# Performance work log

Hardware: AMD Instinct MI355X
Metric: run time of the kernel (lower is better)

Reference implementation:

```python
import jax, jax.numpy as jnp
import numpy as np

EPS_BN = 1e-5
NEG_SLOPE = 0.2

def gat_layer(x, src, dst, N, W, a_src, a_dst, b, heads, ch, concat):
    # x: [N, Fin]; W: [Fin, heads*ch]; a_src/a_dst: [heads, ch]; b: [heads*ch] or [ch]
    xw = (x @ W).reshape(N, heads, ch)                      # [N,H,C]
    al_src = jnp.einsum('nhc,hc->nh', xw, a_src)            # [N,H]
    al_dst = jnp.einsum('nhc,hc->nh', xw, a_dst)
    e = jax.nn.leaky_relu(al_src[src] + al_dst[dst], NEG_SLOPE)  # [E,H]
    m = jax.ops.segment_max(e, dst, num_segments=N)         # segment softmax (stable)
    ee = jnp.exp(e - m[dst])
    s = jax.ops.segment_sum(ee, dst, num_segments=N)
    alpha = ee / (s[dst] + 1e-16)                            # [E,H]
    msg = xw[src] * alpha[:, :, None]                        # [E,H,C]
    out = jax.ops.segment_sum(msg, dst, num_segments=N)      # [N,H,C]
    if concat:
        return out.reshape(N, heads * ch) + b
    return out.mean(axis=1) + b

def setup_inputs():
    key = jax.random.key(0)
    ks = jax.random.split(key, 24)
    N, E, dim_in, dim_out = 20000, 320000, 256, 16
    x = jax.random.normal(ks[0], (N, dim_in), dtype=jnp.float32)
    edge_index = jax.random.randint(ks[1], (2, E), 0, N, dtype=jnp.int64)
    def glorot(k, shape):
        fan = shape[0] + shape[-1]
        return jax.random.uniform(k, shape, jnp.float32, -1.0, 1.0) * np.sqrt(6.0 / fan)
    return {
        'x': x, 'edge_index': edge_index,
        'bn_gamma': jnp.ones((dim_in,), jnp.float32),
        'bn_beta': jnp.zeros((dim_in,), jnp.float32),
        'W1': glorot(ks[2], (dim_in, 16 * 64)),
        'a1_src': glorot(ks[3], (16, 64)), 'a1_dst': glorot(ks[4], (16, 64)),
        'b1': jnp.zeros((16 * 64,), jnp.float32),
        'p1': jnp.float32(0.25),
        'W2': glorot(ks[5], (dim_in + 16 * 64, 8 * 8)),
        'a2_src': glorot(ks[6], (8, 8)), 'a2_dst': glorot(ks[7], (8, 8)),
        'b2': jnp.zeros((8 * 8,), jnp.float32),
        'p2': jnp.float32(0.25),
        'W3': glorot(ks[8], (8 * 8, 8 * dim_out)),
        'a3_src': glorot(ks[9], (8, dim_out)), 'a3_dst': glorot(ks[10], (8, dim_out)),
        'b3': jnp.zeros((dim_out,), jnp.float32),
    }

def reference(x, edge_index, bn_gamma, bn_beta, W1, a1_src, a1_dst, b1, p1,
              W2, a2_src, a2_dst, b2, p2, W3, a3_src, a3_dst, b3):
    N = x.shape[0]
    # PyG GATConv default add_self_loops=True
    loops = jnp.arange(N, dtype=edge_index.dtype)
    src = jnp.concatenate([edge_index[0], loops])
    dst = jnp.concatenate([edge_index[1], loops])
    # BatchNorm1d (training-mode batch stats)
    mu = x.mean(axis=0)
    var = x.var(axis=0)
    x_in = (x - mu) * jax.lax.rsqrt(var + EPS_BN) * bn_gamma + bn_beta
    h = gat_layer(x_in, src, dst, N, W1, a1_src, a1_dst, b1, 16, 64, True)
    h = jnp.where(h >= 0, h, p1 * h)  # PReLU
    h = gat_layer(jnp.concatenate([x_in, h], axis=1), src, dst, N, W2, a2_src, a2_dst, b2, 8, 8, True)
    h = jnp.where(h >= 0, h, p2 * h)
    h = gat_layer(h, src, dst, N, W3, a3_src, a3_dst, b3, 8, b3.shape[0], False)
    return jax.nn.log_softmax(h, axis=1)
```

## Files before the change

kernel.cpp:

```cpp
#include <hip/hip_runtime.h>
#include <math.h>

typedef unsigned int u32;
typedef unsigned short u16;
typedef u32 u32x4 __attribute__((ext_vector_type(4)));
typedef float f32x4 __attribute__((ext_vector_type(4)));

__device__ __forceinline__ u16 f2bf(float f) {
  u32 u = __builtin_bit_cast(u32, f);
  return (u16)((u + 0x7FFFu + ((u >> 16) & 1u)) >> 16);
}
__device__ __forceinline__ float bf2f(u32 lo16) {
  return __builtin_bit_cast(float, lo16 << 16);
}
__device__ __forceinline__ void mfma16(f32x4& c, const u32x4& a, const u32x4& b) {
  asm volatile("v_mfma_f32_16x16x32_bf16 %0, %1, %2, %0" : "+v"(c) : "v"(a), "v"(b));
}
__device__ __forceinline__ float lrelu(float e) { return fmaxf(e, 0.2f * e); }

__global__ void prep1_kernel(const float* __restrict__ x, float* __restrict__ musum,
                             float* __restrict__ sqsum, const int* __restrict__ ei, int E,
                             int N, int* __restrict__ cnt) {
  int b = blockIdx.x;
  int t = threadIdx.x;
  if (b < 256) {
    float s = 0.f, s2 = 0.f;
    for (int r = b; r < N; r += 256) {
      float v = x[(size_t)r * 256 + t];
      s += v;
      s2 += v * v;
    }
    atomicAdd(&musum[t], s);
    atomicAdd(&sqsum[t], s2);
  } else {
    int e = (b - 256) * 256 + t;
    int ET = E + N;
    if (e < ET) {
      int d = (e < E) ? ei[E + e] : (e - E);
      atomicAdd(&cnt[d], 1);
    }
  }
}

__global__ __launch_bounds__(1024) void prep2_kernel(
    int* __restrict__ cnt, int* __restrict__ row_ptr, int* __restrict__ perm,
    const float* __restrict__ x, const float* __restrict__ musum,
    const float* __restrict__ sqsum, const float* __restrict__ gamma,
    const float* __restrict__ beta, u16* __restrict__ xin, int N, float invN) {
  int t = threadIdx.x;
  if (blockIdx.x == 0) {
    __shared__ int part[1024];
    __shared__ int bins[256];
    __shared__ int bs[256];
    int chunk = (N + 1023) / 1024;
    int lo = min(t * chunk, N);
    int hi = min(lo + chunk, N);
    if (t < 256) bins[t] = 0;
    __syncthreads();
    int s = 0;
    for (int i = lo; i < hi; i++) {
      int d = cnt[i];
      s += d;
      atomicAdd(&bins[min(d, 255)], 1);
    }
    part[t] = s;
    __syncthreads();
    for (int off = 1; off < 1024; off <<= 1) {
      int v = (t >= off) ? part[t - off] : 0;
      __syncthreads();
      part[t] += v;
      __syncthreads();
    }
    if (t < 256) bs[t] = bins[t];
    __syncthreads();
    for (int off = 1; off < 256; off <<= 1) {
      int v = (t < 256 && t >= off) ? bs[t - off] : 0;
      __syncthreads();
      if (t < 256) bs[t] += v;
      __syncthreads();
    }
    if (t < 256) bins[t] = (t == 0) ? 0 : bs[t - 1];
    __syncthreads();
    for (int i = lo; i < hi; i++) {
      int d = min(cnt[i], 255);
      int pos = atomicAdd(&bins[d], 1);
      perm[pos] = i;
    }
    __syncthreads();
    int run = (t == 0) ? 0 : part[t - 1];
    for (int i = lo; i < hi; i++) {
      int d = cnt[i];
      row_ptr[i] = run;
      cnt[i] = run;
      run += d;
    }
    if (t == 1023) row_ptr[N] = part[1023];
  } else {
    int col = t & 255, ro = t >> 8;
    float mu = musum[col] * invN;
    float var = sqsum[col] * invN - mu * mu;
    float sc = gamma[col] * rsqrtf(var + 1e-5f);
    float sh = beta[col] - mu * sc;
    for (int r = (blockIdx.x - 1) * 4 + ro; r < N; r += 256 * 4) {
      size_t idx = (size_t)r * 256 + col;
      xin[idx] = f2bf(x[idx] * sc + sh);
    }
  }
}

__global__ void prep3_kernel(const int* __restrict__ ei, int E, int N, int FILLB,
                             int* __restrict__ cursor, int* __restrict__ csr_src,
                             const float* __restrict__ W1, const float* __restrict__ a1s,
                             const float* __restrict__ a1d, const float* __restrict__ W2,
                             const float* __restrict__ a2s, const float* __restrict__ a2d,
                             const float* __restrict__ W3, const float* __restrict__ a3s,
                             const float* __restrict__ a3d, u16* __restrict__ Wt1,
                             u16* __restrict__ Wt2, u16* __restrict__ Wt3) {
  int b = blockIdx.x;
  if (b < FILLB) {
    int e = b * 256 + threadIdx.x;
    int ET = E + N;
    if (e < ET) {
      int s, d;
      if (e < E) { s = ei[e]; d = ei[E + e]; }
      else       { s = e - E; d = s; }
      int pos = atomicAdd(&cursor[d], 1);
      csr_src[pos] = s;
    }
    return;
  }
  const int S1 = 1024 * 256, S2 = 64 * 1280, S3 = 128 * 64;
  const int A1 = 32 * 256, A2 = 16 * 1280, A3 = 16 * 64;
  const int Z1 = 96 * 256, Z2 = 16 * 1280, Z3 = 16 * 64;
  int o = (b - FILLB) * 256 + threadIdx.x;
  if (o < S1) {
    int n = o / 256, k = o % 256;
    Wt1[o] = f2bf(W1[(size_t)k * 1024 + n]);
    return;
  }
  o -= S1;
  if (o < S2) {
    int n = o / 1280, k = o % 1280;
    Wt2[o] = f2bf(W2[(size_t)k * 64 + n]);
    return;
  }
  o -= S2;
  if (o < S3) {
    int n = o / 64, k = o % 64;
    Wt3[o] = f2bf(W3[(size_t)k * 128 + n]);
    return;
  }
  o -= S3;
  if (o < A1) {
    int jj = o / 256, k = o % 256, h = jj >> 1;
    const float* av = (jj & 1) ? a1d : a1s;
    float s = 0.f;
    for (int c = 0; c < 64; c++) s += W1[(size_t)k * 1024 + h * 64 + c] * av[h * 64 + c];
    Wt1[(size_t)(1024 + jj) * 256 + k] = f2bf(s);
    return;
  }
  o -= A1;
  if (o < A2) {
    int jj = o / 1280, k = o % 1280, h = jj >> 1;
    const float* av = (jj & 1) ? a2d : a2s;
    float s = 0.f;
    for (int c = 0; c < 8; c++) s += W2[(size_t)k * 64 + h * 8 + c] * av[h * 8 + c];
    Wt2[(size_t)(64 + jj) * 1280 + k] = f2bf(s);
    return;
  }
  o -= A2;
  if (o < A3) {
    int jj = o / 64, k = o % 64, h = jj >> 1;
    const float* av = (jj & 1) ? a3d : a3s;
    float s = 0.f;
    for (int c = 0; c < 16; c++) s += W3[(size_t)k * 128 + h * 16 + c] * av[h * 16 + c];
    Wt3[(size_t)(128 + jj) * 64 + k] = f2bf(s);
    return;
  }
  o -= A3;
  if (o < Z1) { Wt1[1056 * 256 + o] = 0; return; }
  o -= Z1;
  if (o < Z2) { Wt2[80 * 1280 + o] = 0; return; }
  o -= Z2;
  if (o < Z3) { Wt3[144 * 64 + o] = 0; return; }
}

template <int BM, int BN, int FM, int FN>
__global__ __launch_bounds__(256) void mfma_gemm_al(
    const u16* __restrict__ A1, const u16* __restrict__ A2, int K1, int K,
    const u16* __restrict__ Wt, u16* __restrict__ Ch, int NcH,
    float* __restrict__ als, float* __restrict__ ald, int ALN, int ALP, int M) {
  constexpr int BK = 32;
  constexpr int ACH = (BM * BK) / 8;
  constexpr int BCH = (BN * BK) / 8;
  static_assert(BM == 2 * FM * 16 && BN == 2 * FN * 16, "wave grid 2x2");
  __shared__ u16 As[2][BM * BK];
  __shared__ u16 Bs[2][BN * BK];
  int t = threadIdx.x;
  int m0 = blockIdx.x * BM, n0 = blockIdx.y * BN;
  int r = t & 15;
  int g = (t >> 4) & 3;
  int wid = t >> 6;
  int wm0 = (wid >> 1) * (FM * 16);
  int wn0 = (wid & 1) * (FN * 16);
  int K8 = K >> 3;
  int K2 = K - K1;

  auto stage = [&](int buf, int k0) {
    const u16* Aseg;
    int sA, kl;
    if (k0 < K1) { Aseg = A1; sA = K1; kl = k0; }
    else         { Aseg = A2; sA = K2; kl = k0 - K1; }
#pragma unroll
    for (int i = 0; i < (ACH + 255) / 256; i++) {
      int c = i * 256 + t;
      if (ACH % 256 == 0 || c < ACH) {
        int m = c >> 2, kb = c & 3;
        __builtin_amdgcn_global_load_lds(
            (const __attribute__((address_space(1))) void*)(Aseg + (size_t)(m0 + m) * sA + kl + kb * 8),
            (__attribute__((address_space(3))) void*)(&As[buf][c * 8]), 16, 0, 0);
      }
    }
#pragma unroll
    for (int i = 0; i < (BCH + 255) / 256; i++) {
      int c = i * 256 + t;
      if (BCH % 256 == 0 || c < BCH) {
        int nn = c >> 2, kb = c & 3;
        __builtin_amdgcn_global_load_lds(
            (const __attribute__((address_space(1))) void*)(Wt + ((size_t)(n0 + nn) * K8 + (k0 >> 3) + kb) * 8),
            (__attribute__((address_space(3))) void*)(&Bs[buf][c * 8]), 16, 0, 0);
      }
    }
  };

  f32x4 acc[FM][FN] = {};
  asm volatile("s_nop 7\n\ts_nop 7" :::);

  stage(0, 0);
  __syncthreads();
  int nt = K / BK;
  for (int ts = 0; ts < nt; ts++) {
    if (ts + 1 < nt) stage((ts + 1) & 1, (ts + 1) * BK);
    int cur = ts & 1;
    u32x4 af[FM], bfr[FN];
#pragma unroll
    for (int fi = 0; fi < FM; fi++)
      af[fi] = *(const u32x4*)(&As[cur][((wm0 + fi * 16 + r) * 4 + g) * 8]);
#pragma unroll
    for (int fj = 0; fj < FN; fj++)
      bfr[fj] = *(const u32x4*)(&Bs[cur][((wn0 + fj * 16 + r) * 4 + g) * 8]);
#pragma unroll
    for (int fi = 0; fi < FM; fi++)
#pragma unroll
      for (int fj = 0; fj < FN; fj++) mfma16(acc[fi][fj], af[fi], bfr[fj]);
    __syncthreads();
  }
  asm volatile("s_nop 7\n\ts_nop 7" :::);

#pragma unroll
  for (int fi = 0; fi < FM; fi++) {
#pragma unroll
    for (int fj = 0; fj < FN; fj++) {
#pragma unroll
      for (int v = 0; v < 4; v++) {
        int m = m0 + wm0 + fi * 16 + g * 4 + v;
        int nn = n0 + wn0 + fj * 16 + r;
        if (m < M) {
          float val = acc[fi][fj][v];
          if (nn < NcH) {
            Ch[(size_t)m * NcH + nn] = f2bf(val);
          } else {
            int j = nn - NcH;
            if (j < ALN) ((j & 1) ? ald : als)[(size_t)(j >> 1) * ALP + m] = val;
          }
        }
      }
    }
  }
}

__global__ __launch_bounds__(256) void gat_agg1_gs(
    const u16* __restrict__ xwh, const float* __restrict__ alsrc,
    const float* __restrict__ aldst, const int* __restrict__ row_ptr,
    const int* __restrict__ csr_src, const int* __restrict__ perm,
    const float* __restrict__ bias, const float* __restrict__ slope_p,
    u16* __restrict__ out, int N, int ALP, int NBH) {
  constexpr int U = 4;
  int b = blockIdx.x;
  int xcd = b & 7, seq = b >> 3;
  int phase = seq / NBH, nb = seq - phase * NBH;
  int h = xcd + (phase << 3);
  int lane = threadIdx.x & 63;
  int g = lane >> 3, l8 = lane & 7;
  int ti = nb * 32 + (threadIdx.x >> 6) * 8 + g;
  int n = perm[min(ti, N - 1)];
  const float* alh = alsrc + (size_t)h * ALP;
  float ad = aldst[(size_t)h * ALP + n];
  int start = row_ptr[n];
  int end = row_ptr[n + 1];
  int deg = (ti < N) ? end - start : 0;
  int endm1 = end - 1;

  float m = -1e30f, s = 0.f;
  float acc[8] = {};
  const u16* base = xwh + (size_t)h * 64 + (size_t)l8 * 8;

  auto fma8 = [&](const u32x4& v, float w) {
#pragma unroll
    for (int i = 0; i < 4; i++) {
      u32 u = v[i];
      acc[2 * i] = fmaf(w, bf2f(u & 0xffffu), acc[2 * i]);
      acc[2 * i + 1] = fmaf(w, bf2f(u >> 16), acc[2 * i + 1]);
    }
  };

  int c[U];
#pragma unroll
  for (int i = 0; i < U; i++) c[i] = csr_src[min(start + i, endm1)];
  int j = 0;
  for (; j + U <= deg; j += U) {
    u32x4 v[U];
    float e[U];
#pragma unroll
    for (int i = 0; i < U; i++) v[i] = *(const u32x4*)(base + (size_t)c[i] * 1024);
#pragma unroll
    for (int i = 0; i < U; i++) e[i] = lrelu(alh[c[i]] + ad);
#pragma unroll
    for (int i = 0; i < U; i++) c[i] = csr_src[min(start + j + U + i, endm1)];
    float mn = fmaxf(fmaxf(e[0], e[1]), fmaxf(e[2], e[3]));
    if (mn > m) {
      float sc = __expf(m - mn);
      s *= sc;
#pragma unroll
      for (int k = 0; k < 8; k++) acc[k] *= sc;
      m = mn;
    }
#pragma unroll
    for (int i = 0; i < U; i++) {
      float w = __expf(e[i] - m);
      s += w;
      fma8(v[i], w);
    }
  }
  for (int i = 0; j < deg; j++, i++) {
    u32x4 v = *(const u32x4*)(base + (size_t)c[i] * 1024);
    float e = lrelu(alh[c[i]] + ad);
    if (e > m) {
      float sc = __expf(m - e);
      s *= sc;
#pragma unroll
      for (int k = 0; k < 8; k++) acc[k] *= sc;
      m = e;
    }
    float w = __expf(e - m);
    s += w;
    fma8(v, w);
  }
  float rr = 1.f / (s + 1e-16f);

  if (ti < N) {
    float p = slope_p[0];
    u32 ow[4];
#pragma unroll
    for (int i = 0; i < 4; i++) {
      int cc = h * 64 + l8 * 8 + 2 * i;
      float v0 = acc[2 * i] * rr + bias[cc];
      float v1 = acc[2 * i + 1] * rr + bias[cc + 1];
      v0 = (v0 >= 0.f) ? v0 : p * v0;
      v1 = (v1 >= 0.f) ? v1 : p * v1;
      ow[i] = (u32)f2bf(v0) | ((u32)f2bf(v1) << 16);
    }
    *(u32x4*)(out + (size_t)n * 1024 + h * 64 + l8 * 8) = *(u32x4*)ow;
  }
}

__global__ __launch_bounds__(256) void gat_agg2_gs(
    const u16* __restrict__ xwh, const float* __restrict__ alsrc,
    const float* __restrict__ aldst, const int* __restrict__ row_ptr,
    const int* __restrict__ csr_src, const int* __restrict__ perm,
    const float* __restrict__ bias, const float* __restrict__ slope_p,
    u16* __restrict__ out, int N, int ALP) {
  constexpr int U = 4;
  int lane = threadIdx.x & 63;
  int g = lane >> 3, l8 = lane & 7;
  int ti = blockIdx.x * 32 + (threadIdx.x >> 6) * 8 + g;
  int n = perm[min(ti, N - 1)];
  const float* alh = alsrc + (size_t)l8 * ALP;
  float ad = aldst[(size_t)l8 * ALP + n];
  int start = row_ptr[n];
  int end = row_ptr[n + 1];
  int deg = (ti < N) ? end - start : 0;
  int endm1 = end - 1;

  float m = -1e30f, s = 0.f;
  float acc[8] = {};
  const u16* base = xwh + (size_t)l8 * 8;

  auto fma8 = [&](const u32x4& v, float w) {
#pragma unroll
    for (int i = 0; i < 4; i++) {
      u32 u = v[i];
      acc[2 * i] = fmaf(w, bf2f(u & 0xffffu), acc[2 * i]);
      acc[2 * i + 1] = fmaf(w, bf2f(u >> 16), acc[2 * i + 1]);
    }
  };

  int c[U];
#pragma unroll
  for (int i = 0; i < U; i++) c[i] = csr_src[min(start + i, endm1)];
  int j = 0;
  for (; j + U <= deg; j += U) {
    u32x4 v[U];
    float e[U];
#pragma unroll
    for (int i = 0; i < U; i++) v[i] = *(const u32x4*)(base + (size_t)c[i] * 64);
#pragma unroll
    for (int i = 0; i < U; i++) e[i] = lrelu(alh[c[i]] + ad);
#pragma unroll
    for (int i = 0; i < U; i++) c[i] = csr_src[min(start + j + U + i, endm1)];
    float mn = fmaxf(fmaxf(e[0], e[1]), fmaxf(e[2], e[3]));
    if (mn > m) {
      float sc = __expf(m - mn);
      s *= sc;
#pragma unroll
      for (int k = 0; k < 8; k++) acc[k] *= sc;
      m = mn;
    }
#pragma unroll
    for (int i = 0; i < U; i++) {
      float w = __expf(e[i] - m);
      s += w;
      fma8(v[i], w);
    }
  }
  for (int i = 0; j < deg; j++, i++) {
    u32x4 v = *(const u32x4*)(base + (size_t)c[i] * 64);
    float e = lrelu(alh[c[i]] + ad);
    if (e > m) {
      float sc = __expf(m - e);
      s *= sc;
#pragma unroll
      for (int k = 0; k < 8; k++) acc[k] *= sc;
      m = e;
    }
    float w = __expf(e - m);
    s += w;
    fma8(v, w);
  }
  float rr = 1.f / (s + 1e-16f);

  if (ti < N) {
    float p = slope_p[0];
    u32 ow[4];
#pragma unroll
    for (int i = 0; i < 4; i++) {
      int cc = l8 * 8 + 2 * i;
      float v0 = acc[2 * i] * rr + bias[cc];
      float v1 = acc[2 * i + 1] * rr + bias[cc + 1];
      v0 = (v0 >= 0.f) ? v0 : p * v0;
      v1 = (v1 >= 0.f) ? v1 : p * v1;
      ow[i] = (u32)f2bf(v0) | ((u32)f2bf(v1) << 16);
    }
    *(u32x4*)(out + (size_t)n * 64 + l8 * 8) = *(u32x4*)ow;
  }
}

__global__ __launch_bounds__(256) void gat_agg3_gs(
    const u16* __restrict__ xwh, const float* __restrict__ alsrc,
    const float* __restrict__ aldst, const int* __restrict__ row_ptr,
    const int* __restrict__ csr_src, const int* __restrict__ perm,
    const float* __restrict__ bias, float* __restrict__ out, int N, int ALP) {
  constexpr int U = 4;
  int lane = threadIdx.x & 63;
  int g = lane >> 4, l16 = lane & 15;
  int head = l16 >> 1;
  int ti = blockIdx.x * 16 + (threadIdx.x >> 6) * 4 + g;
  int n = perm[min(ti, N - 1)];
  const float* alh = alsrc + (size_t)head * ALP;
  float ad = aldst[(size_t)head * ALP + n];
  int start = row_ptr[n];
  int end = row_ptr[n + 1];
  int deg = (ti < N) ? end - start : 0;
  int endm1 = end - 1;

  float m = -1e30f, s = 0.f;
  float acc[8] = {};
  const u16* base = xwh + (size_t)l16 * 8;

  auto fma8 = [&](const u32x4& v, float w) {
#pragma unroll
    for (int i = 0; i < 4; i++) {
      u32 u = v[i];
      acc[2 * i] = fmaf(w, bf2f(u & 0xffffu), acc[2 * i]);
      acc[2 * i + 1] = fmaf(w, bf2f(u >> 16), acc[2 * i + 1]);
    }
  };

  int c[U];
#pragma unroll
  for (int i = 0; i < U; i++) c[i] = csr_src[min(start + i, endm1)];
  int j = 0;
  for (; j + U <= deg; j += U) {
    u32x4 v[U];
    float e[U];
#pragma unroll
    for (int i = 0; i < U; i++) v[i] = *(const u32x4*)(base + (size_t)c[i] * 128);
#pragma unroll
    for (int i = 0; i < U; i++) e[i] = lrelu(alh[c[i]] + ad);
#pragma unroll
    for (int i = 0; i < U; i++) c[i] = csr_src[min(start + j + U + i, endm1)];
    float mn = fmaxf(fmaxf(e[0], e[1]), fmaxf(e[2], e[3]));
    if (mn > m) {
      float sc = __expf(m - mn);
      s *= sc;
#pragma unroll
      for (int k = 0; k < 8; k++) acc[k] *= sc;
      m = mn;
    }
#pragma unroll
    for (int i = 0; i < U; i++) {
      float w = __expf(e[i] - m);
      s += w;
      fma8(v[i], w);
    }
  }
  for (int i = 0; j < deg; j++, i++) {
    u32x4 v = *(const u32x4*)(base + (size_t)c[i] * 128);
    float e = lrelu(alh[c[i]] + ad);
    if (e > m) {
      float sc = __expf(m - e);
      s *= sc;
#pragma unroll
      for (int k = 0; k < 8; k++) acc[k] *= sc;
      m = e;
    }
    float w = __expf(e - m);
    s += w;
    fma8(v, w);
  }
  float rr = 1.f / (s + 1e-16f);
#pragma unroll
  for (int k = 0; k < 8; k++) acc[k] *= rr;

#pragma unroll
  for (int st = 2; st <= 8; st <<= 1)
#pragma unroll
    for (int k = 0; k < 8; k++) acc[k] += __shfl_xor(acc[k], st);

  int half = l16 & 1;
  float v8[8];
  float mx = -1e30f;
#pragma unroll
  for (int k = 0; k < 8; k++) {
    v8[k] = acc[k] * 0.125f + bias[half * 8 + k];
    mx = fmaxf(mx, v8[k]);
  }
  mx = fmaxf(mx, __shfl_xor(mx, 1));
  float se = 0.f;
#pragma unroll
  for (int k = 0; k < 8; k++) se += __expf(v8[k] - mx);
  se += __shfl_xor(se, 1);
  float lse = mx + logf(se);
  if (ti < N && l16 < 2) {
    float4 o0 = make_float4(v8[0] - lse, v8[1] - lse, v8[2] - lse, v8[3] - lse);
    float4 o1 = make_float4(v8[4] - lse, v8[5] - lse, v8[6] - lse, v8[7] - lse);
    float* op = out + (size_t)n * 16 + half * 8;
    *(float4*)op = o0;
    *(float4*)(op + 4) = o1;
  }
}

extern "C" void kernel_launch(void* const* d_in, const int* in_sizes, int n_in,
                              void* d_out, int out_size, void* d_ws, size_t ws_size,
                              hipStream_t stream) {
  const float* x        = (const float*)d_in[0];
  const int*   ei       = (const int*)d_in[1];
  const float* bn_gamma = (const float*)d_in[2];
  const float* bn_beta  = (const float*)d_in[3];
  const float* W1       = (const float*)d_in[4];
  const float* a1s      = (const float*)d_in[5];
  const float* a1d      = (const float*)d_in[6];
  const float* b1       = (const float*)d_in[7];
  const float* p1       = (const float*)d_in[8];
  const float* W2       = (const float*)d_in[9];
  const float* a2s      = (const float*)d_in[10];
  const float* a2d      = (const float*)d_in[11];
  const float* b2       = (const float*)d_in[12];
  const float* p2       = (const float*)d_in[13];
  const float* W3       = (const float*)d_in[14];
  const float* a3s      = (const float*)d_in[15];
  const float* a3d      = (const float*)d_in[16];
  const float* b3       = (const float*)d_in[17];
  float* out = (float*)d_out;

  const int F  = in_sizes[2];
  const int N  = in_sizes[0] / F;
  const int E  = in_sizes[1] / 2;
  const int ET = E + N;
  const int MP = ((N + 127) / 128) * 128;

  size_t off = 0;
  auto alloc = [&](size_t bytes) -> char* {
    char* r = (char*)d_ws + off;
    off += (bytes + 255) & ~(size_t)255;
    return r;
  };
  float* musum   = (float*)alloc(F * 4);
  float* sqsum   = (float*)alloc(F * 4);
  int*   cursor  = (int*)alloc((size_t)N * 4);
  int*   row_ptr = (int*)alloc((size_t)(N + 1) * 4);
  int*   csr_src = (int*)alloc((size_t)ET * 4);
  int*   perm    = (int*)alloc((size_t)N * 4);
  float* al_s    = (float*)alloc((size_t)16 * MP * 4);
  float* al_d    = (float*)alloc((size_t)16 * MP * 4);
  u16*   Wt1     = (u16*)alloc((size_t)1152 * 256 * 2);
  u16*   Wt2     = (u16*)alloc((size_t)96 * 1280 * 2);
  u16*   Wt3     = (u16*)alloc((size_t)160 * 64 * 2);
  u16*   x_in_h  = (u16*)alloc((size_t)MP * 256 * 2);
  u16*   xw1h    = (u16*)alloc((size_t)MP * 1024 * 2);
  u16*   h1      = (u16*)alloc((size_t)MP * 1024 * 2);
  u16*   xw2h    = (u16*)alloc((size_t)MP * 64 * 2);
  u16*   h2h     = (u16*)alloc((size_t)MP * 64 * 2);
  u16*   xw3h    = (u16*)alloc((size_t)MP * 128 * 2);

  hipMemsetAsync(musum, 0, (size_t)2 * F * 4 + (size_t)N * 4, stream);

  int CNTB = (ET + 255) / 256;
  prep1_kernel<<<256 + CNTB, 256, 0, stream>>>(x, musum, sqsum, ei, E, N, cursor);

  prep2_kernel<<<257, 1024, 0, stream>>>(cursor, row_ptr, perm, x, musum, sqsum, bn_gamma,
                                         bn_beta, x_in_h, N, 1.0f / (float)N);

  {
    int total_wt = 1024 * 256 + 64 * 1280 + 128 * 64
                 + 32 * 256 + 16 * 1280 + 16 * 64
                 + 96 * 256 + 16 * 1280 + 16 * 64;
    int WTB = (total_wt + 255) / 256;
    prep3_kernel<<<CNTB + WTB, 256, 0, stream>>>(ei, E, N, CNTB, cursor, csr_src, W1, a1s, a1d,
                                                 W2, a2s, a2d, W3, a3s, a3d, Wt1, Wt2, Wt3);
  }

  {
    dim3 grid(MP / 128, 9);
    mfma_gemm_al<128, 128, 4, 4><<<grid, 256, 0, stream>>>(
        x_in_h, x_in_h, 256, 256, Wt1, xw1h, 1024, al_s, al_d, 32, MP, N);
    int NBH = (N + 31) / 32;
    gat_agg1_gs<<<8 * NBH * 2, 256, 0, stream>>>(xw1h, al_s, al_d, row_ptr, csr_src, perm, b1, p1,
                                                 h1, N, MP, NBH);
  }

  {
    dim3 grid((N + 63) / 64, 1);
    mfma_gemm_al<64, 96, 2, 3><<<grid, 256, 0, stream>>>(
        x_in_h, h1, 256, 1280, Wt2, xw2h, 64, al_s, al_d, 16, MP, N);
    gat_agg2_gs<<<(N + 31) / 32, 256, 0, stream>>>(xw2h, al_s, al_d, row_ptr, csr_src, perm, b2,
                                                   p2, h2h, N, MP);
  }

  {
    dim3 grid((N + 63) / 64, 1);
    mfma_gemm_al<64, 160, 2, 5><<<grid, 256, 0, stream>>>(
        h2h, h2h, 64, 64, Wt3, xw3h, 128, al_s, al_d, 16, MP, N);
    gat_agg3_gs<<<(N + 15) / 16, 256, 0, stream>>>(xw3h, al_s, al_d, row_ptr, csr_src, perm, b3,
                                                   out, N, MP);
  }
}
```

Before: 307.8 us.

## Parameterize GEMM K-tile, shrink layer-2 M-tile, use packed FMA in aggregation

```diff
diff --git a/kernel.cpp b/kernel.cpp
--- a/kernel.cpp
+++ b/kernel.cpp
@@ -5,16 +5,23 @@
 typedef unsigned short u16;
 typedef u32 u32x4 __attribute__((ext_vector_type(4)));
 typedef float f32x4 __attribute__((ext_vector_type(4)));
+typedef float f32x2 __attribute__((ext_vector_type(2)));
 
 __device__ __forceinline__ u16 f2bf(float f) {
   u32 u = __builtin_bit_cast(u32, f);
   return (u16)((u + 0x7FFFu + ((u >> 16) & 1u)) >> 16);
 }
-__device__ __forceinline__ float bf2f(u32 lo16) {
-  return __builtin_bit_cast(float, lo16 << 16);
-}
 __device__ __forceinline__ void mfma16(f32x4& c, const u32x4& a, const u32x4& b) {
   asm volatile("v_mfma_f32_16x16x32_bf16 %0, %1, %2, %0" : "+v"(c) : "v"(a), "v"(b));
+}
+__device__ __forceinline__ void pkfma(f32x2& acc, f32x2 val, f32x2 w) {
+  asm volatile("v_pk_fma_f32 %0, %1, %2, %0" : "+v"(acc) : "v"(val), "v"(w));
+}
+__device__ __forceinline__ f32x2 unpk(u32 u) {
+  f32x2 v;
+  v.x = __builtin_bit_cast(float, u << 16);
+  v.y = __builtin_bit_cast(float, u & 0xffff0000u);
+  return v;
 }
 __device__ __forceinline__ float lrelu(float e) { return fmaxf(e, 0.2f * e); }
 
@@ -185,12 +192,12 @@
   if (o < Z3) { Wt3[144 * 64 + o] = 0; return; }
 }
 
-template <int BM, int BN, int FM, int FN>
+template <int BM, int BN, int FM, int FN, int BK>
 __global__ __launch_bounds__(256) void mfma_gemm_al(
     const u16* __restrict__ A1, const u16* __restrict__ A2, int K1, int K,
     const u16* __restrict__ Wt, u16* __restrict__ Ch, int NcH,
     float* __restrict__ als, float* __restrict__ ald, int ALN, int ALP, int M) {
-  constexpr int BK = 32;
+  constexpr int KC8 = BK / 8;
   constexpr int ACH = (BM * BK) / 8;
   constexpr int BCH = (BN * BK) / 8;
   static_assert(BM == 2 * FM * 16 && BN == 2 * FN * 16, "wave grid 2x2");
@@ -215,7 +222,7 @@
     for (int i = 0; i < (ACH + 255) / 256; i++) {
       int c = i * 256 + t;
       if (ACH % 256 == 0 || c < ACH) {
-        int m = c >> 2, kb = c & 3;
+        int m = c / KC8, kb = c % KC8;
         __builtin_amdgcn_global_load_lds(
             (const __attribute__((address_space(1))) void*)(Aseg + (size_t)(m0 + m) * sA + kl + kb * 8),
             (__attribute__((address_space(3))) void*)(&As[buf][c * 8]), 16, 0, 0);
@@ -225,7 +232,7 @@
     for (int i = 0; i < (BCH + 255) / 256; i++) {
       int c = i * 256 + t;
       if (BCH % 256 == 0 || c < BCH) {
-        int nn = c >> 2, kb = c & 3;
+        int nn = c / KC8, kb = c % KC8;
         __builtin_amdgcn_global_load_lds(
             (const __attribute__((address_space(1))) void*)(Wt + ((size_t)(n0 + nn) * K8 + (k0 >> 3) + kb) * 8),
             (__attribute__((address_space(3))) void*)(&Bs[buf][c * 8]), 16, 0, 0);
@@ -242,17 +249,20 @@
   for (int ts = 0; ts < nt; ts++) {
     if (ts + 1 < nt) stage((ts + 1) & 1, (ts + 1) * BK);
     int cur = ts & 1;
-    u32x4 af[FM], bfr[FN];
-#pragma unroll
-    for (int fi = 0; fi < FM; fi++)
-      af[fi] = *(const u32x4*)(&As[cur][((wm0 + fi * 16 + r) * 4 + g) * 8]);
-#pragma unroll
-    for (int fj = 0; fj < FN; fj++)
-      bfr[fj] = *(const u32x4*)(&Bs[cur][((wn0 + fj * 16 + r) * 4 + g) * 8]);
-#pragma unroll
-    for (int fi = 0; fi < FM; fi++)
-#pragma unroll
-      for (int fj = 0; fj < FN; fj++) mfma16(acc[fi][fj], af[fi], bfr[fj]);
+#pragma unroll
+    for (int ks = 0; ks < BK / 32; ks++) {
+      u32x4 af[FM], bfr[FN];
+#pragma unroll
+      for (int fi = 0; fi < FM; fi++)
+        af[fi] = *(const u32x4*)(&As[cur][((wm0 + fi * 16 + r) * KC8 + ks * 4 + g) * 8]);
+#pragma unroll
+      for (int fj = 0; fj < FN; fj++)
+        bfr[fj] = *(const u32x4*)(&Bs[cur][((wn0 + fj * 16 + r) * KC8 + ks * 4 + g) * 8]);
+#pragma unroll
+      for (int fi = 0; fi < FM; fi++)
+#pragma unroll
+        for (int fj = 0; fj < FN; fj++) mfma16(acc[fi][fj], af[fi], bfr[fj]);
+    }
     __syncthreads();
   }
   asm volatile("s_nop 7\n\ts_nop 7" :::);
@@ -302,16 +312,15 @@
   int endm1 = end - 1;
 
   float m = -1e30f, s = 0.f;
-  float acc[8] = {};
+  f32x2 acc2[4] = {};
   const u16* base = xwh + (size_t)h * 64 + (size_t)l8 * 8;
 
   auto fma8 = [&](const u32x4& v, float w) {
-#pragma unroll
-    for (int i = 0; i < 4; i++) {
-      u32 u = v[i];
-      acc[2 * i] = fmaf(w, bf2f(u & 0xffffu), acc[2 * i]);
-      acc[2 * i + 1] = fmaf(w, bf2f(u >> 16), acc[2 * i + 1]);
-    }
+    f32x2 w2;
+    w2.x = w;
+    w2.y = w;
+#pragma unroll
+    for (int i = 0; i < 4; i++) pkfma(acc2[i], unpk(v[i]), w2);
   };
 
   int c[U];
@@ -332,7 +341,7 @@
       float sc = __expf(m - mn);
       s *= sc;
 #pragma unroll
-      for (int k = 0; k < 8; k++) acc[k] *= sc;
+      for (int k = 0; k < 4; k++) acc2[k] *= sc;
       m = mn;
     }
 #pragma unroll
@@ -349,7 +358,7 @@
       float sc = __expf(m - e);
       s *= sc;
 #pragma unroll
-      for (int k = 0; k < 8; k++) acc[k] *= sc;
+      for (int k = 0; k < 4; k++) acc2[k] *= sc;
       m = e;
     }
     float w = __expf(e - m);
@@ -364,8 +373,8 @@
 #pragma unroll
     for (int i = 0; i < 4; i++) {
       int cc = h * 64 + l8 * 8 + 2 * i;
-      float v0 = acc[2 * i] * rr + bias[cc];
-      float v1 = acc[2 * i + 1] * rr + bias[cc + 1];
+      float v0 = acc2[i].x * rr + bias[cc];
+      float v1 = acc2[i].y * rr + bias[cc + 1];
       v0 = (v0 >= 0.f) ? v0 : p * v0;
       v1 = (v1 >= 0.f) ? v1 : p * v1;
       ow[i] = (u32)f2bf(v0) | ((u32)f2bf(v1) << 16);
@@ -393,16 +402,15 @@
   int endm1 = end - 1;
 
   float m = -1e30f, s = 0.f;
-  float acc[8] = {};
+  f32x2 acc2[4] = {};
   const u16* base = xwh + (size_t)l8 * 8;
 
   auto fma8 = [&](const u32x4& v, float w) {
-#pragma unroll
-    for (int i = 0; i < 4; i++) {
-      u32 u = v[i];
-      acc[2 * i] = fmaf(w, bf2f(u & 0xffffu), acc[2 * i]);
-      acc[2 * i + 1] = fmaf(w, bf2f(u >> 16), acc[2 * i + 1]);
-    }
+    f32x2 w2;
+    w2.x = w;
+    w2.y = w;
+#pragma unroll
+    for (int i = 0; i < 4; i++) pkfma(acc2[i], unpk(v[i]), w2);
   };
 
   int c[U];
@@ -423,7 +431,7 @@
       float sc = __expf(m - mn);
       s *= sc;
 #pragma unroll
-      for (int k = 0; k < 8; k++) acc[k] *= sc;
+      for (int k = 0; k < 4; k++) acc2[k] *= sc;
       m = mn;
     }
 #pragma unroll
@@ -440,7 +448,7 @@
       float sc = __expf(m - e);
       s *= sc;
 #pragma unroll
-      for (int k = 0; k < 8; k++) acc[k] *= sc;
+      for (int k = 0; k < 4; k++) acc2[k] *= sc;
       m = e;
     }
     float w = __expf(e - m);
@@ -455,8 +463,8 @@
 #pragma unroll
     for (int i = 0; i < 4; i++) {
       int cc = l8 * 8 + 2 * i;
-      float v0 = acc[2 * i] * rr + bias[cc];
-      float v1 = acc[2 * i + 1] * rr + bias[cc + 1];
+      float v0 = acc2[i].x * rr + bias[cc];
+      float v1 = acc2[i].y * rr + bias[cc + 1];
       v0 = (v0 >= 0.f) ? v0 : p * v0;
       v1 = (v1 >= 0.f) ? v1 : p * v1;
       ow[i] = (u32)f2bf(v0) | ((u32)f2bf(v1) << 16);
@@ -484,16 +492,15 @@
   int endm1 = end - 1;
 
   float m = -1e30f, s = 0.f;
-  float acc[8] = {};
+  f32x2 acc2[4] = {};
   const u16* base = xwh + (size_t)l16 * 8;
 
   auto fma8 = [&](const u32x4& v, float w) {
-#pragma unroll
-    for (int i = 0; i < 4; i++) {
-      u32 u = v[i];
-      acc[2 * i] = fmaf(w, bf2f(u & 0xffffu), acc[2 * i]);
-      acc[2 * i + 1] = fmaf(w, bf2f(u >> 16), acc[2 * i + 1]);
-    }
+    f32x2 w2;
+    w2.x = w;
+    w2.y = w;
+#pragma unroll
+    for (int i = 0; i < 4; i++) pkfma(acc2[i], unpk(v[i]), w2);
   };
 
   int c[U];
@@ -514,7 +521,7 @@
       float sc = __expf(m - mn);
       s *= sc;
 #pragma unroll
-      for (int k = 0; k < 8; k++) acc[k] *= sc;
+      for (int k = 0; k < 4; k++) acc2[k] *= sc;
       m = mn;
     }
 #pragma unroll
@@ -531,7 +538,7 @@
       float sc = __expf(m - e);
       s *= sc;
 #pragma unroll
-      for (int k = 0; k < 8; k++) acc[k] *= sc;
+      for (int k = 0; k < 4; k++) acc2[k] *= sc;
       m = e;
     }
     float w = __expf(e - m);
@@ -539,20 +546,25 @@
     fma8(v, w);
   }
   float rr = 1.f / (s + 1e-16f);
-#pragma unroll
-  for (int k = 0; k < 8; k++) acc[k] *= rr;
+
+  float a8[8];
+#pragma unroll
+  for (int k = 0; k < 4; k++) {
+    a8[2 * k] = acc2[k].x * rr;
+    a8[2 * k + 1] = acc2[k].y * rr;
+  }
 
 #pragma unroll
   for (int st = 2; st <= 8; st <<= 1)
 #pragma unroll
-    for (int k = 0; k < 8; k++) acc[k] += __shfl_xor(acc[k], st);
+    for (int k = 0; k < 8; k++) a8[k] += __shfl_xor(a8[k], st);
 
   int half = l16 & 1;
   float v8[8];
   float mx = -1e30f;
 #pragma unroll
   for (int k = 0; k < 8; k++) {
-    v8[k] = acc[k] * 0.125f + bias[half * 8 + k];
+    v8[k] = a8[k] * 0.125f + bias[half * 8 + k];
     mx = fmaxf(mx, v8[k]);
   }
   mx = fmaxf(mx, __shfl_xor(mx, 1));
@@ -642,7 +654,7 @@
 
   {
     dim3 grid(MP / 128, 9);
-    mfma_gemm_al<128, 128, 4, 4><<<grid, 256, 0, stream>>>(
+    mfma_gemm_al<128, 128, 4, 4, 32><<<grid, 256, 0, stream>>>(
         x_in_h, x_in_h, 256, 256, Wt1, xw1h, 1024, al_s, al_d, 32, MP, N);
     int NBH = (N + 31) / 32;
     gat_agg1_gs<<<8 * NBH * 2, 256, 0, stream>>>(xw1h, al_s, al_d, row_ptr, csr_src, perm, b1, p1,
@@ -650,8 +662,8 @@
   }
 
   {
-    dim3 grid((N + 63) / 64, 1);
-    mfma_gemm_al<64, 96, 2, 3><<<grid, 256, 0, stream>>>(
+    dim3 grid((N + 31) / 32, 1);
+    mfma_gemm_al<32, 96, 1, 3, 64><<<grid, 256, 0, stream>>>(
         x_in_h, h1, 256, 1280, Wt2, xw2h, 64, al_s, al_d, 16, MP, N);
     gat_agg2_gs<<<(N + 31) / 32, 256, 0, stream>>>(xw2h, al_s, al_d, row_ptr, csr_src, perm, b2,
                                                    p2, h2h, N, MP);
@@ -659,7 +671,7 @@
 
   {
     dim3 grid((N + 63) / 64, 1);
-    mfma_gemm_al<64, 160, 2, 5><<<grid, 256, 0, stream>>>(
+    mfma_gemm_al<64, 160, 2, 5, 64><<<grid, 256, 0, stream>>>(
         h2h, h2h, 64, 64, Wt3, xw3h, 128, al_s, al_d, 16, MP, N);
     gat_agg3_gs<<<(N + 15) / 16, 256, 0, stream>>>(xw3h, al_s, al_d, row_ptr, csr_src, perm, b3,
                                                    out, N, MP);
```

New measurement: 303.3 us (median of 2 runs). No clear change (-1.4%).
